# Performance work log

Hardware: AMD Instinct MI355X
Metric: run time of the kernel (lower is better)

The kernel has to match this reference:

```python
import jax, jax.numpy as jnp
import numpy as np

B = 8192
D_S, D_W, D_P, D_E, D_C, D_Z = 1024, 1024, 512, 1024, 512, 512
H_P = 2 * D_P          # particle hidden_dim default
RANK = D_W // 4        # low-rank A factor
EPS = 1e-5             # torch LayerNorm default eps


def _ln(x, g, b):
    m = jnp.mean(x, axis=-1, keepdims=True)
    v = jnp.var(x, axis=-1, keepdims=True)
    return (x - m) * jax.lax.rsqrt(v + EPS) * g + b


def setup_inputs() -> dict:
    key = jax.random.key(0)
    ks = iter(jax.random.split(key, 48))
    def randn(shape, scale=1.0):
        return jax.random.normal(next(ks), shape, dtype=jnp.float32) * scale
    def lin(dout, din):  # torch Linear: W [out,in], b [out]
        s = 1.0 / np.sqrt(din)
        return randn((dout, din), s), randn((dout,), s)
    inp = {}
    inp["s_prev"] = randn((B, D_S))
    inp["w_prev"] = randn((B, D_W))
    inp["p_prev"] = randn((B, D_P))
    inp["e_t"] = randn((B, D_E))
    inp["c_t"] = randn((B, D_C))
    d_in = D_S + D_E + D_C
    # fusion_net: Linear -> LN -> ReLU -> Linear
    inp["fw1"], inp["fb1"] = lin(2 * D_Z, d_in)
    inp["fln_g"] = jnp.ones((2 * D_Z,), jnp.float32)
    inp["fln_b"] = jnp.zeros((2 * D_Z,), jnp.float32)
    inp["fw2"], inp["fb2"] = lin(D_Z, 2 * D_Z)
    # wave subsystem
    inp["A_diag"] = jnp.zeros((D_W,), jnp.float32)
    inp["A_U"] = randn((D_W, RANK), 0.01)
    inp["A_V"] = randn((D_W, RANK), 0.01)
    inp["amod_w"], inp["amod_b"] = lin(D_W, D_C)
    inp["bnet_w"], inp["bnet_b"] = lin(D_W, D_C + D_Z)
    # particle subsystem phi
    inp["pw1"], inp["pb1"] = lin(H_P, D_P + D_Z + D_C)
    inp["pln_g"] = jnp.ones((H_P,), jnp.float32)
    inp["pln_b"] = jnp.zeros((H_P,), jnp.float32)
    inp["pw2"], inp["pb2"] = lin(H_P // 2, H_P)
    inp["pw3"], inp["pb3"] = lin(D_P, H_P // 2)
    # gate + mixing projections + output norm
    inp["gw"], inp["gb"] = lin(D_S, d_in)
    inp["uw"] = randn((D_S, D_W), 1.0 / np.sqrt(D_W))
    inp["up"] = randn((D_S, D_P), 1.0 / np.sqrt(D_P))
    inp["oln_g"] = jnp.ones((D_S,), jnp.float32)
    inp["oln_b"] = jnp.zeros((D_S,), jnp.float32)
    return inp


def reference(s_prev, w_prev, p_prev, e_t, c_t,
              fw1, fb1, fln_g, fln_b, fw2, fb2,
              A_diag, A_U, A_V, amod_w, amod_b, bnet_w, bnet_b,
              pw1, pb1, pln_g, pln_b, pw2, pb2, pw3, pb3,
              gw, gb, uw, up, oln_g, oln_b):
    # fusion: z_t = Linear(ReLU(LN(Linear([s||e||c]))))
    fin = jnp.concatenate([s_prev, e_t, c_t], axis=-1)      # [B, d_s+d_e+d_c]
    h = jax.nn.relu(_ln(fin @ fw1.T + fb1, fln_g, fln_b))
    z_t = h @ fw2.T + fb2                                   # [B, d_z]
    # wave: A = (diag(tanh(A_diag)*0.9) + A_U A_V^T) * mod[None,:]
    # so (A w)[b,i] = sum_j A_base[i,j] * (mod*w)[b,j] -> (mod*w) @ A_base^T
    A_base = jnp.diag(jnp.tanh(A_diag) * 0.9) + A_U @ A_V.T  # [d_w, d_w]
    mod = jnp.tanh(c_t @ amod_w.T + amod_b)                  # [B, d_w]
    w_linear = (mod * w_prev) @ A_base.T
    b_in = jnp.concatenate([c_t, z_t], axis=-1)
    w_t = w_linear + b_in @ bnet_w.T + bnet_b                # [B, d_w]
    # particle: p_t = p_prev + tanh(MLP([p||z||c]))
    pin = jnp.concatenate([p_prev, z_t, c_t], axis=-1)
    h1 = jax.nn.relu(_ln(pin @ pw1.T + pb1, pln_g, pln_b))
    h2 = jax.nn.relu(h1 @ pw2.T + pb2)
    p_t = p_prev + jnp.tanh(h2 @ pw3.T + pb3)                # [B, d_p]
    # gated mixing
    g_t = jax.nn.sigmoid(fin @ gw.T + gb)                    # [B, d_s]
    s_t = s_prev + g_t * (p_t @ up.T) + (1.0 - g_t) * (w_t @ uw.T)
    s_t = _ln(s_t, oln_g, oln_b)
    return (s_t, w_t, p_t)
```

## Files before the change

kernel.cpp:

```cpp
#include <hip/hip_runtime.h>
#include <math.h>

typedef unsigned short u16;
typedef __attribute__((ext_vector_type(8))) short short8;
typedef __attribute__((ext_vector_type(4))) float f32x4;

#define AS1C(p) ((const __attribute__((address_space(1))) void*)(p))
#define AS3(p)  ((__attribute__((address_space(3))) void*)(p))

static __device__ __forceinline__ float b2f(u16 h) {
    union { unsigned u; float f; } c; c.u = ((unsigned)h) << 16; return c.f;
}
static __device__ __forceinline__ u16 f2b(float f) {
    union { float f; unsigned u; } c; c.f = f;
    unsigned r = c.u + 0x7FFFu + ((c.u >> 16) & 1u);
    return (u16)(r >> 16);
}

#define EP_NONE     0
#define EP_RELU     1
#define EP_SIGMOID  2
#define EP_TANH_MUL 3
#define EP_TANH_ADD 4
#define EP_DIAG     5

struct GDesc {
    const u16* A;
    const u16* W;
    const float* bias;
    const float* auxf;
    u16* outb;
    float* outf;
    int lda, ldd, N, K, ep, nbm;
};

struct GArgs { GDesc d0, d1, d2; int s1, s2; };

__global__ __launch_bounds__(512, 2)
void gemm_q(GArgs ga)
{
    __shared__ __align__(16) u16 LDS[65536];

    const int bid = (int)blockIdx.x;
    GDesc dd = (bid < ga.s1) ? ga.d0 : ((bid < ga.s2) ? ga.d1 : ga.d2);
    const int b = bid - ((bid < ga.s1) ? 0 : ((bid < ga.s2) ? ga.s1 : ga.s2));

    const int tid  = threadIdx.x;
    const int lane = tid & 63;
    const int wid  = tid >> 6;
    const int wr   = wid >> 2;
    const int wc   = wid & 3;

    const int bm = b % dd.nbm;
    const int bn = b / dd.nbm;
    const int lda = dd.lda, K = dd.K, N = dd.N, ldd = dd.ldd;
    const int nkt = K >> 6;

    const int srow  = tid >> 3;
    const int sslot = tid & 7;
    const int sgcol = (sslot ^ (srow & 7)) * 8;
    const u16* Ag = dd.A + (size_t)(bm * 256 + srow) * lda + sgcol;
    const u16* Wg = dd.W + (size_t)(bn * 256 + srow) * K + sgcol;
    const int ldst = tid * 8;

    f32x4 acc[8][4];
#pragma unroll
    for (int m = 0; m < 8; ++m)
#pragma unroll
        for (int n = 0; n < 4; ++n) acc[m][n] = (f32x4){0.f, 0.f, 0.f, 0.f};

#define STAGE(bufi, kt)                                                          \
    {                                                                            \
        const int k0_ = (kt) << 6;                                               \
        u16* al_ = &LDS[(bufi) * 32768 + ldst];                                  \
        u16* bl_ = &LDS[(bufi) * 32768 + 16384 + ldst];                          \
        _Pragma("unroll")                                                        \
        for (int j = 0; j < 4; ++j)                                              \
            __builtin_amdgcn_global_load_lds(AS1C(Ag + (size_t)(j * 64) * lda + k0_), \
                                             AS3(al_ + j * 4096), 16, 0, 0);     \
        _Pragma("unroll")                                                        \
        for (int j = 0; j < 4; ++j)                                              \
            __builtin_amdgcn_global_load_lds(AS1C(Wg + (size_t)(j * 64) * K + k0_),   \
                                             AS3(bl_ + j * 4096), 16, 0, 0);     \
    }

    const int swz  = (lane & 7) << 4;
    const int cnat = (lane >> 4) << 4;

    short8 AF0[4][2], AF1[4][2], BF[2][2];

#define LDA_SET(AF, mh, Al)                                                      \
    {                                                                            \
        const int rb_ = wr * 128 + (mh) * 64 + (lane & 15);                      \
        _Pragma("unroll")                                                        \
        for (int mm = 0; mm < 4; ++mm) {                                         \
            const u16* rp_ = (Al) + (rb_ + mm * 16) * 64;                        \
            _Pragma("unroll")                                                    \
            for (int ks = 0; ks < 2; ++ks)                                       \
                AF[mm][ks] = *(const short8*)(rp_ + ((((ks << 6) | cnat) ^ swz) >> 1)); \
        }                                                                        \
    }

#define LDB_SET(nh, Bl)                                                          \
    {                                                                            \
        const int rb_ = wc * 64 + (nh) * 32 + (lane & 15);                       \
        _Pragma("unroll")                                                        \
        for (int nn = 0; nn < 2; ++nn) {                                         \
            const u16* rp_ = (Bl) + (rb_ + nn * 16) * 64;                        \
            _Pragma("unroll")                                                    \
            for (int ks = 0; ks < 2; ++ks)                                       \
                BF[nn][ks] = *(const short8*)(rp_ + ((((ks << 6) | cnat) ^ swz) >> 1)); \
        }                                                                        \
    }

#define QMFMA(AF, mh, nh)                                                        \
    {                                                                            \
        __builtin_amdgcn_s_setprio(1);                                           \
        _Pragma("unroll")                                                        \
        for (int mm = 0; mm < 4; ++mm)                                           \
            _Pragma("unroll")                                                    \
            for (int nn = 0; nn < 2; ++nn)                                       \
                _Pragma("unroll")                                                \
                for (int ks = 0; ks < 2; ++ks)                                   \
                    acc[(mh) * 4 + mm][(nh) * 2 + nn] =                          \
                        __builtin_amdgcn_mfma_f32_16x16x32_bf16(                 \
                            AF[mm][ks], BF[nn][ks], acc[(mh) * 4 + mm][(nh) * 2 + nn], 0, 0, 0); \
        __builtin_amdgcn_s_setprio(0);                                           \
    }

    STAGE(0, 0);
    __builtin_amdgcn_sched_barrier(0);
    asm volatile("s_waitcnt vmcnt(0)" ::: "memory");
    __builtin_amdgcn_sched_barrier(0);
    __builtin_amdgcn_s_barrier();
    __builtin_amdgcn_sched_barrier(0);

    int buf = 0;
    for (int kt = 0; kt < nkt; ++kt) {
        const int ka = (kt + 1 < nkt) ? kt + 1 : nkt - 1;
        STAGE(buf ^ 1, ka);
        __builtin_amdgcn_sched_barrier(0);

        const u16* Al = &LDS[buf * 32768];
        const u16* Bl = Al + 16384;

        LDA_SET(AF0, 0, Al);
        LDB_SET(0, Bl);
        LDA_SET(AF1, 1, Al);
        QMFMA(AF0, 0, 0);
        QMFMA(AF1, 1, 0);
        LDB_SET(1, Bl);
        QMFMA(AF1, 1, 1);
        QMFMA(AF0, 0, 1);

        __builtin_amdgcn_sched_barrier(0);
        asm volatile("s_waitcnt vmcnt(0)" ::: "memory");
        __builtin_amdgcn_sched_barrier(0);
        __builtin_amdgcn_s_barrier();
        __builtin_amdgcn_sched_barrier(0);
        buf ^= 1;
    }

#undef STAGE
#undef LDA_SET
#undef LDB_SET
#undef QMFMA

    const int rbase = bm * 256 + wr * 128 + (lane >> 4) * 4;
    const int cbase = bn * 256 + wc * 64 + (lane & 15);
    const int ep = dd.ep;
#pragma unroll
    for (int n = 0; n < 4; ++n) {
        const int C = cbase + n * 16;
        const float bv = dd.bias ? dd.bias[C] : 0.f;
#pragma unroll
        for (int m = 0; m < 8; ++m) {
            const int R0 = rbase + m * 16;
#pragma unroll
            for (int j = 0; j < 4; ++j) {
                const int R = R0 + j;
                float v = acc[m][n][j] + bv;
                if (ep == EP_RELU)          v = fmaxf(v, 0.f);
                else if (ep == EP_SIGMOID)  v = 1.f / (1.f + expf(-v));
                else if (ep == EP_TANH_MUL) v = tanhf(v) * dd.auxf[(size_t)R * N + C];
                else if (ep == EP_TANH_ADD) v = dd.auxf[(size_t)R * N + C] + tanhf(v);
                else if (ep == EP_DIAG)     { if (R == C) v += 0.9f * tanhf(dd.auxf[R]); }
                dd.outb[(size_t)R * ldd + C] = f2b(v);
                if (dd.outf) dd.outf[(size_t)R * N + C] = v;
            }
        }
    }
}

template<bool RELU>
__global__ __launch_bounds__(256)
void ln1024(u16* __restrict__ X, const float* __restrict__ gam, const float* __restrict__ bet)
{
    const int row = blockIdx.x;
    u16* xp = X + (size_t)row * 1024 + threadIdx.x * 4;
    u16 loc[4];
    *(uint2*)loc = *(const uint2*)xp;
    float x0 = b2f(loc[0]), x1 = b2f(loc[1]), x2 = b2f(loc[2]), x3 = b2f(loc[3]);
    float s = x0 + x1 + x2 + x3;
    float q = x0 * x0 + x1 * x1 + x2 * x2 + x3 * x3;
#pragma unroll
    for (int off = 32; off; off >>= 1) { s += __shfl_xor(s, off); q += __shfl_xor(q, off); }
    __shared__ float sm[8];
    const int wave = threadIdx.x >> 6, lane = threadIdx.x & 63;
    if (lane == 0) { sm[wave] = s; sm[4 + wave] = q; }
    __syncthreads();
    s = sm[0] + sm[1] + sm[2] + sm[3];
    q = sm[4] + sm[5] + sm[6] + sm[7];
    const float mean = s * (1.f / 1024.f);
    const float var  = q * (1.f / 1024.f) - mean * mean;
    const float inv  = rsqrtf(var + 1e-5f);
    const int cb = threadIdx.x * 4;
#pragma unroll
    for (int j = 0; j < 4; ++j) {
        float y = (b2f(loc[j]) - mean) * inv * gam[cb + j] + bet[cb + j];
        if (RELU) y = fmaxf(y, 0.f);
        loc[j] = f2b(y);
    }
    *(uint2*)xp = *(uint2*)loc;
}

__global__ __launch_bounds__(256)
void mix_ln(const float* __restrict__ sp, const u16* __restrict__ gt,
            const u16* __restrict__ pm, const u16* __restrict__ wm,
            const float* __restrict__ og, const float* __restrict__ ob,
            float* __restrict__ out)
{
    const int row = blockIdx.x;
    const size_t base = (size_t)row * 1024 + threadIdx.x * 4;
    float4 lsp = *(const float4*)(sp + base);
    u16 lg[4], lp[4], lw[4];
    *(uint2*)lg = *(const uint2*)(gt + base);
    *(uint2*)lp = *(const uint2*)(pm + base);
    *(uint2*)lw = *(const uint2*)(wm + base);
    float x[4];
    const float* lspp = (const float*)&lsp;
#pragma unroll
    for (int j = 0; j < 4; ++j) {
        float g = b2f(lg[j]);
        x[j] = lspp[j] + g * b2f(lp[j]) + (1.f - g) * b2f(lw[j]);
    }
    float s = x[0] + x[1] + x[2] + x[3];
    float q = x[0]*x[0] + x[1]*x[1] + x[2]*x[2] + x[3]*x[3];
#pragma unroll
    for (int off = 32; off; off >>= 1) { s += __shfl_xor(s, off); q += __shfl_xor(q, off); }
    __shared__ float sm[8];
    const int wave = threadIdx.x >> 6, lane = threadIdx.x & 63;
    if (lane == 0) { sm[wave] = s; sm[4 + wave] = q; }
    __syncthreads();
    s = sm[0] + sm[1] + sm[2] + sm[3];
    q = sm[4] + sm[5] + sm[6] + sm[7];
    const float mean = s * (1.f / 1024.f);
    const float var  = q * (1.f / 1024.f) - mean * mean;
    const float inv  = rsqrtf(var + 1e-5f);
    const int cb = threadIdx.x * 4;
    float4 o;
    float* op = (float*)&o;
#pragma unroll
    for (int j = 0; j < 4; ++j)
        op[j] = (x[j] - mean) * inv * og[cb + j] + ob[cb + j];
    *(float4*)(out + base) = o;
}

struct CDesc { const void* src; u16* dst; int srcCols8; int dstStride; int dstOff; unsigned end; int isbf16; };
struct CArgs { CDesc d[16]; unsigned total; };

__global__ __launch_bounds__(256)
void multi_copy(CArgs ca)
{
    const unsigned idx = blockIdx.x * 256 + threadIdx.x;
    if (idx >= ca.total) return;
    int i = 0; unsigned start = 0;
    while (idx >= ca.d[i].end) { start = ca.d[i].end; ++i; }
    const CDesc cd = ca.d[i];
    const unsigned local = idx - start;
    const int r = local / cd.srcCols8;
    const int c = local % cd.srcCols8;
    u16 o[8];
    if (cd.isbf16) {
        *(uint4*)o = *(const uint4*)((const u16*)cd.src + ((size_t)r * cd.srcCols8 + c) * 8);
    } else {
        const float* s = (const float*)cd.src + ((size_t)r * cd.srcCols8 + c) * 8;
        const float4 a = *(const float4*)s;
        const float4 bq = *(const float4*)(s + 4);
        const float* ap = (const float*)&a;
        const float* bp = (const float*)&bq;
#pragma unroll
        for (int j = 0; j < 4; ++j) { o[j] = f2b(ap[j]); o[4 + j] = f2b(bp[j]); }
    }
    *(uint4*)(cd.dst + (size_t)r * cd.dstStride + cd.dstOff + (size_t)c * 8) = *(uint4*)o;
}

extern "C" void kernel_launch(void* const* d_in, const int* in_sizes, int n_in,
                              void* d_out, int out_size, void* d_ws, size_t ws_size,
                              hipStream_t stream)
{
    const float* s_prev = (const float*)d_in[0];
    const float* w_prev = (const float*)d_in[1];
    const float* p_prev = (const float*)d_in[2];
    const float* e_t    = (const float*)d_in[3];
    const float* c_t    = (const float*)d_in[4];
    const float* fw1    = (const float*)d_in[5];
    const float* fb1    = (const float*)d_in[6];
    const float* fln_g  = (const float*)d_in[7];
    const float* fln_b  = (const float*)d_in[8];
    const float* fw2    = (const float*)d_in[9];
    const float* fb2    = (const float*)d_in[10];
    const float* A_diag = (const float*)d_in[11];
    const float* A_U    = (const float*)d_in[12];
    const float* A_V    = (const float*)d_in[13];
    const float* amod_w = (const float*)d_in[14];
    const float* amod_b = (const float*)d_in[15];
    const float* bnet_w = (const float*)d_in[16];
    const float* bnet_b = (const float*)d_in[17];
    const float* pw1    = (const float*)d_in[18];
    const float* pb1    = (const float*)d_in[19];
    const float* pln_g  = (const float*)d_in[20];
    const float* pln_b  = (const float*)d_in[21];
    const float* pw2    = (const float*)d_in[22];
    const float* pb2    = (const float*)d_in[23];
    const float* pw3    = (const float*)d_in[24];
    const float* pb3    = (const float*)d_in[25];
    const float* gw     = (const float*)d_in[26];
    const float* gb     = (const float*)d_in[27];
    const float* uw     = (const float*)d_in[28];
    const float* up     = (const float*)d_in[29];
    const float* oln_g  = (const float*)d_in[30];
    const float* oln_b  = (const float*)d_in[31];

    float* out_s = (float*)d_out;
    float* out_w = out_s + (size_t)8192 * 1024;
    float* out_p = out_w + (size_t)8192 * 1024;

    u16* ws = (u16*)d_ws;
    u16* FIN  = ws;
    u16* W_bf = ws + 12582912;
    u16* H    = ws + 20971520;
    u16* P_bf = H;
    u16* Z    = ws + 29360128;
    u16* G    = ws + 33554432;
    u16* ACAT = ws + 41943040;
    u16* PM   = ACAT;
    u16* WM   = ACAT + 8388608;
    u16* WCAT = ws + 58720256;
    u16* wb   = ws + 60817408;
    u16* fw1b  = wb;
    u16* gwb   = wb + 2621440;
    u16* fw2b  = wb + 5242880;
    u16* amodb = wb + 5767168;
    u16* pw1b  = wb + 6291456;
    u16* pw2b  = wb + 7864320;
    u16* pw3b  = wb + 8388608;
    u16* uwb   = wb + 8650752;
    u16* upb   = wb + 9699328;
    u16* AUb   = wb + 10223616;
    u16* AVb   = wb + 10485760;

    const dim3 blk(256);
    const dim3 blk512(512);

    {
        CArgs ca; unsigned cum = 0; int nd = 0;
        auto push = [&](const void* src, u16* dst, int cols8, int stride, int off,
                        int rows, int isbf) {
            cum += (unsigned)rows * cols8;
            ca.d[nd++] = CDesc{src, dst, cols8, stride, off, cum, isbf};
        };
        push(fw1,    fw1b,  320, 2560, 0,    1024, 0);
        push(gw,     gwb,   320, 2560, 0,    1024, 0);
        push(fw2,    fw2b,  128, 1024, 0,    512,  0);
        push(amod_w, amodb, 64,  512,  0,    1024, 0);
        push(pw1,    pw1b,  192, 1536, 0,    1024, 0);
        push(pw2,    pw2b,  128, 1024, 0,    512,  0);
        push(pw3,    pw3b,  64,  512,  0,    512,  0);
        push(uw,     uwb,   128, 1024, 0,    1024, 0);
        push(up,     upb,   64,  512,  0,    1024, 0);
        push(A_U,    AUb,   32,  256,  0,    1024, 0);
        push(A_V,    AVb,   32,  256,  0,    1024, 0);
        push(s_prev, FIN,   128, 2560, 0,    8192, 0);
        push(e_t,    FIN,   128, 2560, 1024, 8192, 0);
        push(c_t,    FIN,   64,  2560, 2048, 8192, 0);
        push(c_t,    ACAT,  64,  2048, 1024, 8192, 0);
        push(bnet_w, WCAT,  128, 2048, 1024, 1024, 0);
        ca.total = cum;
        multi_copy<<<dim3((cum + 255) / 256), blk, 0, stream>>>(ca);
    }

    {
        GArgs ga;
        ga.d0 = GDesc{FIN, fw1b, fb1, nullptr, H, nullptr, 2560, 1024, 1024, 2560, EP_NONE,    32};
        ga.d1 = GDesc{FIN, gwb,  gb,  nullptr, G, nullptr, 2560, 1024, 1024, 2560, EP_SIGMOID, 32};
        ga.d2 = ga.d1; ga.s1 = 128; ga.s2 = 256;
        gemm_q<<<dim3(256), blk512, 0, stream>>>(ga);
    }
    ln1024<true><<<8192, blk, 0, stream>>>(H, fln_g, fln_b);

    {
        GArgs ga;
        ga.d0 = GDesc{H,          fw2b,  fb2,     nullptr, Z,    nullptr, 1024, 512,  512,  1024, EP_NONE,     32};
        ga.d1 = GDesc{FIN + 2048, amodb, amod_b,  w_prev,  ACAT, nullptr, 2560, 2048, 1024, 512,  EP_TANH_MUL, 32};
        ga.d2 = GDesc{AUb,        AVb,   nullptr, A_diag,  WCAT, nullptr, 256,  2048, 1024, 256,  EP_DIAG,     4};
        ga.s1 = 64; ga.s2 = 192;
        gemm_q<<<dim3(208), blk512, 0, stream>>>(ga);
    }

    {
        CArgs ca; unsigned cum = 0; int nd = 0;
        auto push = [&](const void* src, u16* dst, int cols8, int stride, int off,
                        int rows, int isbf) {
            cum += (unsigned)rows * cols8;
            ca.d[nd++] = CDesc{src, dst, cols8, stride, off, cum, isbf};
        };
        push(p_prev, FIN,  64, 1536, 0,    8192, 0);
        push(Z,      FIN,  64, 1536, 512,  8192, 1);
        push(c_t,    FIN,  64, 1536, 1024, 8192, 0);
        push(Z,      ACAT, 64, 2048, 1536, 8192, 1);
        ca.total = cum;
        multi_copy<<<dim3((cum + 255) / 256), blk, 0, stream>>>(ca);
    }

    {
        GArgs ga;
        ga.d0 = GDesc{ACAT, WCAT, bnet_b, nullptr, W_bf, out_w,   2048, 1024, 1024, 2048, EP_NONE, 32};
        ga.d1 = GDesc{FIN,  pw1b, pb1,    nullptr, H,    nullptr, 1536, 1024, 1024, 1536, EP_NONE, 32};
        ga.d2 = ga.d1; ga.s1 = 128; ga.s2 = 256;
        gemm_q<<<dim3(256), blk512, 0, stream>>>(ga);
    }
    ln1024<true><<<8192, blk, 0, stream>>>(H, pln_g, pln_b);

    {
        GArgs ga;
        ga.d0 = GDesc{H,    pw2b, pb2,     nullptr, Z,  nullptr, 1024, 512,  512,  1024, EP_RELU, 32};
        ga.d1 = GDesc{W_bf, uwb,  nullptr, nullptr, WM, nullptr, 1024, 1024, 1024, 1024, EP_NONE, 32};
        ga.d2 = ga.d1; ga.s1 = 64; ga.s2 = 192;
        gemm_q<<<dim3(192), blk512, 0, stream>>>(ga);
    }

    {
        GArgs ga;
        ga.d0 = GDesc{Z, pw3b, pb3, p_prev, P_bf, out_p, 512, 512, 512, 512, EP_TANH_ADD, 32};
        ga.d1 = ga.d0; ga.d2 = ga.d0; ga.s1 = 64; ga.s2 = 64;
        gemm_q<<<dim3(64), blk512, 0, stream>>>(ga);
    }

    {
        GArgs ga;
        ga.d0 = GDesc{P_bf, upb, nullptr, nullptr, PM, nullptr, 512, 1024, 1024, 512, EP_NONE, 32};
        ga.d1 = ga.d0; ga.d2 = ga.d0; ga.s1 = 128; ga.s2 = 128;
        gemm_q<<<dim3(128), blk512, 0, stream>>>(ga);
    }

    mix_ln<<<8192, blk, 0, stream>>>(s_prev, G, PM, WM, oln_g, oln_b, out_s);
}
```

Measured before the change: 557.8 us.

## Interleave half-tile global-to-LDS loads with MFMA quadrants in GEMM

Splits each K-tile's global-to-LDS stage into four half-stages (A and B, each in two halves) and issues them between the four MFMA quadrant phases. Partial vmcnt(4) waits plus barriers replace the single full drain at the end of each iteration. Warp-to-tile row and column mapping is remapped so each half-stage feeds a contiguous 128-row quadrant, and the epilogue indexing is adjusted to match. The aim is to overlap memory latency with compute more finely, at the cost of three barriers per K iteration and more delicate buffer-hazard ordering.

```diff
diff --git a/kernel.cpp b/kernel.cpp
--- a/kernel.cpp
+++ b/kernel.cpp
@@ -37,7 +37,7 @@
 struct GArgs { GDesc d0, d1, d2; int s1, s2; };
 
 __global__ __launch_bounds__(512, 2)
-void gemm_q(GArgs ga)
+void gemm_8p(GArgs ga)
 {
     __shared__ __align__(16) u16 LDS[65536];
 
@@ -69,19 +69,32 @@
 #pragma unroll
         for (int n = 0; n < 4; ++n) acc[m][n] = (f32x4){0.f, 0.f, 0.f, 0.f};
 
-#define STAGE(bufi, kt)                                                          \
+#define STAGE_AH(bufi, kt, h)                                                    \
     {                                                                            \
         const int k0_ = (kt) << 6;                                               \
-        u16* al_ = &LDS[(bufi) * 32768 + ldst];                                  \
-        u16* bl_ = &LDS[(bufi) * 32768 + 16384 + ldst];                          \
+        u16* d_ = &LDS[(bufi) * 32768 + ldst];                                   \
         _Pragma("unroll")                                                        \
-        for (int j = 0; j < 4; ++j)                                              \
+        for (int j = 2 * (h); j < 2 * (h) + 2; ++j)                              \
             __builtin_amdgcn_global_load_lds(AS1C(Ag + (size_t)(j * 64) * lda + k0_), \
-                                             AS3(al_ + j * 4096), 16, 0, 0);     \
+                                             AS3(d_ + j * 4096), 16, 0, 0);      \
+    }
+#define STAGE_BH(bufi, kt, h)                                                    \
+    {                                                                            \
+        const int k0_ = (kt) << 6;                                               \
+        u16* d_ = &LDS[(bufi) * 32768 + 16384 + ldst];                           \
         _Pragma("unroll")                                                        \
-        for (int j = 0; j < 4; ++j)                                              \
+        for (int j = 2 * (h); j < 2 * (h) + 2; ++j)                              \
             __builtin_amdgcn_global_load_lds(AS1C(Wg + (size_t)(j * 64) * K + k0_),   \
-                                             AS3(bl_ + j * 4096), 16, 0, 0);     \
+                                             AS3(d_ + j * 4096), 16, 0, 0);      \
+    }
+
+#define VWAIT4()                                                                 \
+    {                                                                            \
+        __builtin_amdgcn_sched_barrier(0);                                       \
+        asm volatile("s_waitcnt vmcnt(4)" ::: "memory");                         \
+        __builtin_amdgcn_sched_barrier(0);                                       \
+        __builtin_amdgcn_s_barrier();                                            \
+        __builtin_amdgcn_sched_barrier(0);                                       \
     }
 
     const int swz  = (lane & 7) << 4;
@@ -91,7 +104,7 @@
 
 #define LDA_SET(AF, mh, Al)                                                      \
     {                                                                            \
-        const int rb_ = wr * 128 + (mh) * 64 + (lane & 15);                      \
+        const int rb_ = (mh) * 128 + wr * 64 + (lane & 15);                      \
         _Pragma("unroll")                                                        \
         for (int mm = 0; mm < 4; ++mm) {                                         \
             const u16* rp_ = (Al) + (rb_ + mm * 16) * 64;                        \
@@ -100,10 +113,9 @@
                 AF[mm][ks] = *(const short8*)(rp_ + ((((ks << 6) | cnat) ^ swz) >> 1)); \
         }                                                                        \
     }
-
 #define LDB_SET(nh, Bl)                                                          \
     {                                                                            \
-        const int rb_ = wc * 64 + (nh) * 32 + (lane & 15);                       \
+        const int rb_ = (nh) * 128 + wc * 32 + (lane & 15);                      \
         _Pragma("unroll")                                                        \
         for (int nn = 0; nn < 2; ++nn) {                                         \
             const u16* rp_ = (Bl) + (rb_ + nn * 16) * 64;                        \
@@ -112,7 +124,6 @@
                 BF[nn][ks] = *(const short8*)(rp_ + ((((ks << 6) | cnat) ^ swz) >> 1)); \
         }                                                                        \
     }
-
 #define QMFMA(AF, mh, nh)                                                        \
     {                                                                            \
         __builtin_amdgcn_s_setprio(1);                                           \
@@ -128,54 +139,56 @@
         __builtin_amdgcn_s_setprio(0);                                           \
     }
 
-    STAGE(0, 0);
-    __builtin_amdgcn_sched_barrier(0);
-    asm volatile("s_waitcnt vmcnt(0)" ::: "memory");
-    __builtin_amdgcn_sched_barrier(0);
-    __builtin_amdgcn_s_barrier();
-    __builtin_amdgcn_sched_barrier(0);
+    STAGE_AH(0, 0, 0);
+    STAGE_BH(0, 0, 0);
+    STAGE_AH(0, 0, 1);
+    STAGE_BH(0, 0, 1);
 
     int buf = 0;
     for (int kt = 0; kt < nkt; ++kt) {
         const int ka = (kt + 1 < nkt) ? kt + 1 : nkt - 1;
-        STAGE(buf ^ 1, ka);
-        __builtin_amdgcn_sched_barrier(0);
-
         const u16* Al = &LDS[buf * 32768];
         const u16* Bl = Al + 16384;
-
+        const int nb = buf ^ 1;
+
+        VWAIT4();
         LDA_SET(AF0, 0, Al);
         LDB_SET(0, Bl);
+        STAGE_AH(nb, ka, 0);
+        QMFMA(AF0, 0, 0);
+
+        VWAIT4();
         LDA_SET(AF1, 1, Al);
-        QMFMA(AF0, 0, 0);
+        STAGE_BH(nb, ka, 0);
         QMFMA(AF1, 1, 0);
+
+        VWAIT4();
         LDB_SET(1, Bl);
+        STAGE_AH(nb, ka, 1);
         QMFMA(AF1, 1, 1);
+
+        __builtin_amdgcn_sched_barrier(0);
+        STAGE_BH(nb, ka, 1);
         QMFMA(AF0, 0, 1);
 
-        __builtin_amdgcn_sched_barrier(0);
-        asm volatile("s_waitcnt vmcnt(0)" ::: "memory");
-        __builtin_amdgcn_sched_barrier(0);
-        __builtin_amdgcn_s_barrier();
-        __builtin_amdgcn_sched_barrier(0);
         buf ^= 1;
     }
 
-#undef STAGE
+#undef STAGE_AH
+#undef STAGE_BH
+#undef VWAIT4
 #undef LDA_SET
 #undef LDB_SET
 #undef QMFMA
 
-    const int rbase = bm * 256 + wr * 128 + (lane >> 4) * 4;
-    const int cbase = bn * 256 + wc * 64 + (lane & 15);
     const int ep = dd.ep;
 #pragma unroll
     for (int n = 0; n < 4; ++n) {
-        const int C = cbase + n * 16;
+        const int C = bn * 256 + (n >> 1) * 128 + wc * 32 + (n & 1) * 16 + (lane & 15);
         const float bv = dd.bias ? dd.bias[C] : 0.f;
 #pragma unroll
         for (int m = 0; m < 8; ++m) {
-            const int R0 = rbase + m * 16;
+            const int R0 = bm * 256 + (m >> 2) * 128 + wr * 64 + (m & 3) * 16 + ((lane >> 4) << 2);
 #pragma unroll
             for (int j = 0; j < 4; ++j) {
                 const int R = R0 + j;
@@ -395,7 +408,7 @@
         ga.d0 = GDesc{FIN, fw1b, fb1, nullptr, H, nullptr, 2560, 1024, 1024, 2560, EP_NONE,    32};
         ga.d1 = GDesc{FIN, gwb,  gb,  nullptr, G, nullptr, 2560, 1024, 1024, 2560, EP_SIGMOID, 32};
         ga.d2 = ga.d1; ga.s1 = 128; ga.s2 = 256;
-        gemm_q<<<dim3(256), blk512, 0, stream>>>(ga);
+        gemm_8p<<<dim3(256), blk512, 0, stream>>>(ga);
     }
     ln1024<true><<<8192, blk, 0, stream>>>(H, fln_g, fln_b);
 
@@ -405,7 +418,7 @@
         ga.d1 = GDesc{FIN + 2048, amodb, amod_b,  w_prev,  ACAT, nullptr, 2560, 2048, 1024, 512,  EP_TANH_MUL, 32};
         ga.d2 = GDesc{AUb,        AVb,   nullptr, A_diag,  WCAT, nullptr, 256,  2048, 1024, 256,  EP_DIAG,     4};
         ga.s1 = 64; ga.s2 = 192;
-        gemm_q<<<dim3(208), blk512, 0, stream>>>(ga);
+        gemm_8p<<<dim3(208), blk512, 0, stream>>>(ga);
     }
 
     {
@@ -428,7 +441,7 @@
         ga.d0 = GDesc{ACAT, WCAT, bnet_b, nullptr, W_bf, out_w,   2048, 1024, 1024, 2048, EP_NONE, 32};
         ga.d1 = GDesc{FIN,  pw1b, pb1,    nullptr, H,    nullptr, 1536, 1024, 1024, 1536, EP_NONE, 32};
         ga.d2 = ga.d1; ga.s1 = 128; ga.s2 = 256;
-        gemm_q<<<dim3(256), blk512, 0, stream>>>(ga);
+        gemm_8p<<<dim3(256), blk512, 0, stream>>>(ga);
     }
     ln1024<true><<<8192, blk, 0, stream>>>(H, pln_g, pln_b);
 
@@ -437,21 +450,21 @@
         ga.d0 = GDesc{H,    pw2b, pb2,     nullptr, Z,  nullptr, 1024, 512,  512,  1024, EP_RELU, 32};
         ga.d1 = GDesc{W_bf, uwb,  nullptr, nullptr, WM, nullptr, 1024, 1024, 1024, 1024, EP_NONE, 32};
         ga.d2 = ga.d1; ga.s1 = 64; ga.s2 = 192;
-        gemm_q<<<dim3(192), blk512, 0, stream>>>(ga);
+        gemm_8p<<<dim3(192), blk512, 0, stream>>>(ga);
     }
 
     {
         GArgs ga;
         ga.d0 = GDesc{Z, pw3b, pb3, p_prev, P_bf, out_p, 512, 512, 512, 512, EP_TANH_ADD, 32};
         ga.d1 = ga.d0; ga.d2 = ga.d0; ga.s1 = 64; ga.s2 = 64;
-        gemm_q<<<dim3(64), blk512, 0, stream>>>(ga);
+        gemm_8p<<<dim3(64), blk512, 0, stream>>>(ga);
     }
 
     {
         GArgs ga;
         ga.d0 = GDesc{P_bf, upb, nullptr, nullptr, PM, nullptr, 512, 1024, 1024, 512, EP_NONE, 32};
         ga.d1 = ga.d0; ga.d2 = ga.d0; ga.s1 = 128; ga.s2 = 128;
-        gemm_q<<<dim3(128), blk512, 0, stream>>>(ga);
+        gemm_8p<<<dim3(128), blk512, 0, stream>>>(ga);
     }
 
     mix_ln<<<8192, blk, 0, stream>>>(s_prev, G, PM, WM, oln_g, oln_b, out_s);
```

After: 529.5 us. -5.1%, faster.
